# Performance work log

Hardware: AMD Instinct MI355X
Metric: run time of the kernel (lower is better)

The kernel has to match this reference:

```python
import jax, jax.numpy as jnp
import numpy as np

B, S, H = 32, 2048, 1024


def setup_inputs() -> dict:
    key = jax.random.key(0)
    ks = jax.random.split(key, 8)
    scale = 1.0 / np.sqrt(H)
    return {
        "query": jax.random.normal(ks[0], (B, 1, H), dtype=jnp.float32),
        "keys": jax.random.normal(ks[1], (B, S, H), dtype=jnp.float32),
        "Wa_w": jax.random.uniform(ks[2], (H, H), jnp.float32, -scale, scale),
        "Wa_b": jax.random.uniform(ks[3], (H,), jnp.float32, -scale, scale),
        "Ua_w": jax.random.uniform(ks[4], (H, H), jnp.float32, -scale, scale),
        "Ua_b": jax.random.uniform(ks[5], (H,), jnp.float32, -scale, scale),
        "Va_w": jax.random.uniform(ks[6], (1, H), jnp.float32, -scale, scale),
        "Va_b": jax.random.uniform(ks[7], (1,), jnp.float32, -scale, scale),
        "idx": 0,
    }


def reference(query, keys, Wa_w, Wa_b, Ua_w, Ua_b, Va_w, Va_b, idx):
    # torch Linear: y = x @ W.T + b
    q_proj = jnp.einsum("bqh,oh->bqo", query, Wa_w) + Wa_b   # (B,1,H)
    k_proj = jnp.einsum("bsh,oh->bso", keys, Ua_w) + Ua_b    # (B,S,H)
    energy = jnp.tanh(q_proj + k_proj)                        # (B,S,H) broadcast over S
    scores = jnp.einsum("bsh,h->bs", energy, Va_w[0]) + Va_b[0]  # (B,S)
    weights = jax.nn.softmax(scores, axis=-1)[:, None, :]     # (B,1,S)
    context = jnp.einsum("bqs,bsh->bqh", weights, keys)       # (B,1,H)
    return (context, weights)
```

## Files before the change

### kernel.cpp

```cpp
#include <hip/hip_runtime.h>
#include <hip/hip_bf16.h>
#include <math.h>


#define B_ 32
#define S_ 2048
#define H_ 1024
#define M_ (B_ * S_)

typedef __bf16 bf16x8 __attribute__((ext_vector_type(8)));
typedef float floatx4 __attribute__((ext_vector_type(4)));

__device__ inline unsigned bf16_rne(float f) {
  unsigned u = __builtin_bit_cast(unsigned, f);
  return (u + 0x7fffu + ((u >> 16) & 1u)) >> 16;
}
__device__ inline unsigned pk2(float x, float y) {
  return bf16_rne(x) | (bf16_rne(y) << 16);
}

#define GLDS(g, l)                                                    \
  __builtin_amdgcn_global_load_lds(                                   \
      (const __attribute__((address_space(1))) void*)(g),             \
      (__attribute__((address_space(3))) void*)(l), 16, 0, 0)

__global__ __launch_bounds__(256) void convert_kernel(
    const float* __restrict__ src, unsigned short* __restrict__ dst, int n8) {
  const int stride = gridDim.x * 256;
  for (int i = blockIdx.x * 256 + threadIdx.x; i < n8; i += stride) {
    const float4 a = ((const float4*)src)[(size_t)i * 2];
    const float4 b = ((const float4*)src)[(size_t)i * 2 + 1];
    uint4 o;
    o.x = pk2(a.x, a.y); o.y = pk2(a.z, a.w);
    o.z = pk2(b.x, b.y); o.w = pk2(b.z, b.w);
    ((uint4*)dst)[i] = o;
  }
}

__global__ __launch_bounds__(256) void qproj_kernel(
    const float* __restrict__ query, const float* __restrict__ Wa_w,
    const float* __restrict__ Wa_b, const float* __restrict__ Ua_b,
    float* __restrict__ qp) {
  const int b = blockIdx.x >> 2;
  const int os = blockIdx.x & 3;
  const int tid = threadIdx.x;
  const int lane = tid & 63;
  const int w = tid >> 6;
  __shared__ float qsh[H_];
  *(float4*)&qsh[tid * 4] = *(const float4*)(query + b * H_ + tid * 4);
  __syncthreads();
  for (int t = 0; t < 64; ++t) {
    const int o = os * 256 + w * 64 + t;
    const float* wr = Wa_w + (size_t)o * H_;
    float p = 0.f;
#pragma unroll
    for (int j = 0; j < 16; ++j) p += wr[lane + 64 * j] * qsh[lane + 64 * j];
#pragma unroll
    for (int m = 32; m; m >>= 1) p += __shfl_xor(p, m);
    if (lane == 0) qp[b * H_ + o] = p + Wa_b[o] + Ua_b[o];
  }
}

__device__ inline void swizzle_rc(int idx, int& rb, int& cb) {
  cb = (idx >> 3) & 7;
  rb = (idx & 7) | ((idx >> 6) << 3);
}

__global__ __launch_bounds__(256) void scores_bf16_kernel(
    const unsigned short* __restrict__ kbf, const unsigned short* __restrict__ ubf,
    const float* __restrict__ qp, const float* __restrict__ Va_w,
    float* __restrict__ scores) {
  const int tid = threadIdx.x;
  int rb, cb;
  swizzle_rc(blockIdx.x, rb, cb);
  const int row0 = rb * 128, c0 = cb * 128;
  const int bq = row0 >> 11;
  const int lane = tid & 63;
  const int w = tid >> 6;
  const int wm = w >> 1, wn = w & 1;
  const int q4 = lane >> 4, n16 = lane & 15;

  __shared__ __align__(16) unsigned short Asm[128][32];
  __shared__ __align__(16) unsigned short Bsm[128][32];
  __shared__ float red[2][128];

  floatx4 acc[4][4];
#pragma unroll
  for (int i = 0; i < 4; ++i)
#pragma unroll
    for (int j = 0; j < 4; ++j) acc[i][j] = {0.f, 0.f, 0.f, 0.f};

  const int r0a = w * 32;
  const int lr = lane >> 2;
  const int lc = (lane & 3) * 8;
  const unsigned short* gA0 = kbf + (size_t)(row0 + r0a + lr) * H_ + lc;
  const unsigned short* gA1 = kbf + (size_t)(row0 + r0a + 16 + lr) * H_ + lc;
  const unsigned short* gB0 = ubf + (size_t)(c0 + r0a + lr) * H_ + lc;
  const unsigned short* gB1 = ubf + (size_t)(c0 + r0a + 16 + lr) * H_ + lc;
  unsigned short* lA0 = &Asm[r0a][0];
  unsigned short* lA1 = &Asm[r0a + 16][0];
  unsigned short* lB0 = &Bsm[r0a][0];
  unsigned short* lB1 = &Bsm[r0a + 16][0];

  for (int kt = 0; kt < 32; ++kt) {
    const int k0 = kt * 32;
    __syncthreads();
    GLDS(gA0 + k0, lA0);
    GLDS(gA1 + k0, lA1);
    GLDS(gB0 + k0, lB0);
    GLDS(gB1 + k0, lB1);
    __syncthreads();
    bf16x8 af[4], bfr[4];
#pragma unroll
    for (int i = 0; i < 4; ++i)
      af[i] = *(const bf16x8*)&Asm[wm * 64 + i * 16 + n16][q4 * 8];
#pragma unroll
    for (int j = 0; j < 4; ++j)
      bfr[j] = *(const bf16x8*)&Bsm[wn * 64 + j * 16 + n16][q4 * 8];
#pragma unroll
    for (int i = 0; i < 4; ++i)
#pragma unroll
      for (int j = 0; j < 4; ++j)
        acc[i][j] = __builtin_amdgcn_mfma_f32_16x16x32_bf16(af[i], bfr[j], acc[i][j], 0, 0, 0);
  }

  float rsum[4][4];
#pragma unroll
  for (int i = 0; i < 4; ++i)
#pragma unroll
    for (int r = 0; r < 4; ++r) rsum[i][r] = 0.f;
#pragma unroll
  for (int j = 0; j < 4; ++j) {
    const int col = c0 + wn * 64 + j * 16 + n16;
    const float qv = qp[bq * H_ + col];
    const float vv = Va_w[col];
#pragma unroll
    for (int i = 0; i < 4; ++i)
#pragma unroll
      for (int r = 0; r < 4; ++r)
        rsum[i][r] += tanhf(acc[i][j][r] + qv) * vv;
  }
#pragma unroll
  for (int i = 0; i < 4; ++i)
#pragma unroll
    for (int r = 0; r < 4; ++r) {
      float v = rsum[i][r];
      v += __shfl_xor(v, 1);
      v += __shfl_xor(v, 2);
      v += __shfl_xor(v, 4);
      v += __shfl_xor(v, 8);
      rsum[i][r] = v;
    }
  if (n16 == 0) {
#pragma unroll
    for (int i = 0; i < 4; ++i)
#pragma unroll
      for (int r = 0; r < 4; ++r)
        red[wn][wm * 64 + i * 16 + q4 * 4 + r] = rsum[i][r];
  }
  __syncthreads();
  if (tid < 128) atomicAdd(scores + row0 + tid, red[0][tid] + red[1][tid]);
}

__global__ __launch_bounds__(256) void scores_f32_kernel(
    const float* __restrict__ keys, const float* __restrict__ Ua_w,
    const float* __restrict__ qp, const float* __restrict__ Va_w,
    float* __restrict__ scores) {
  const int tid = threadIdx.x;
  int rb, cb;
  swizzle_rc(blockIdx.x, rb, cb);
  const int row0 = rb * 128, c0 = cb * 128;
  const int bq = row0 >> 11;
  const int lane = tid & 63;
  const int w = tid >> 6;
  const int wm = w >> 1, wn = w & 1;
  const int q4 = lane >> 4, n16 = lane & 15;

  __shared__ __align__(16) unsigned short Asm[128][40];
  __shared__ __align__(16) unsigned short Bsm[128][40];
  __shared__ float red[2][128];

  floatx4 acc[4][4];
#pragma unroll
  for (int i = 0; i < 4; ++i)
#pragma unroll
    for (int j = 0; j < 4; ++j) acc[i][j] = {0.f, 0.f, 0.f, 0.f};

  for (int kt = 0; kt < 32; ++kt) {
    const int k0 = kt * 32;
    __syncthreads();
#pragma unroll
    for (int rep = 0; rep < 4; ++rep) {
      const int idx4 = rep * 256 + tid;
      const int r = idx4 >> 3;
      const int c4 = (idx4 & 7) << 2;
      const float4 va = *(const float4*)(keys + (size_t)(row0 + r) * H_ + k0 + c4);
      *(uint2*)&Asm[r][c4] = make_uint2(pk2(va.x, va.y), pk2(va.z, va.w));
      const float4 vb = *(const float4*)(Ua_w + (size_t)(c0 + r) * H_ + k0 + c4);
      *(uint2*)&Bsm[r][c4] = make_uint2(pk2(vb.x, vb.y), pk2(vb.z, vb.w));
    }
    __syncthreads();
    bf16x8 af[4], bfr[4];
#pragma unroll
    for (int i = 0; i < 4; ++i)
      af[i] = *(const bf16x8*)&Asm[wm * 64 + i * 16 + n16][q4 * 8];
#pragma unroll
    for (int j = 0; j < 4; ++j)
      bfr[j] = *(const bf16x8*)&Bsm[wn * 64 + j * 16 + n16][q4 * 8];
#pragma unroll
    for (int i = 0; i < 4; ++i)
#pragma unroll
      for (int j = 0; j < 4; ++j)
        acc[i][j] = __builtin_amdgcn_mfma_f32_16x16x32_bf16(af[i], bfr[j], acc[i][j], 0, 0, 0);
  }

  float rsum[4][4];
#pragma unroll
  for (int i = 0; i < 4; ++i)
#pragma unroll
    for (int r = 0; r < 4; ++r) rsum[i][r] = 0.f;
#pragma unroll
  for (int j = 0; j < 4; ++j) {
    const int col = c0 + wn * 64 + j * 16 + n16;
    const float qv = qp[bq * H_ + col];
    const float vv = Va_w[col];
#pragma unroll
    for (int i = 0; i < 4; ++i)
#pragma unroll
      for (int r = 0; r < 4; ++r)
        rsum[i][r] += tanhf(acc[i][j][r] + qv) * vv;
  }
#pragma unroll
  for (int i = 0; i < 4; ++i)
#pragma unroll
    for (int r = 0; r < 4; ++r) {
      float v = rsum[i][r];
      v += __shfl_xor(v, 1);
      v += __shfl_xor(v, 2);
      v += __shfl_xor(v, 4);
      v += __shfl_xor(v, 8);
      rsum[i][r] = v;
    }
  if (n16 == 0) {
#pragma unroll
    for (int i = 0; i < 4; ++i)
#pragma unroll
      for (int r = 0; r < 4; ++r)
        red[wn][wm * 64 + i * 16 + q4 * 4 + r] = rsum[i][r];
  }
  __syncthreads();
  if (tid < 128) atomicAdd(scores + row0 + tid, red[0][tid] + red[1][tid]);
}

__global__ __launch_bounds__(256) void softmax_kernel(float* __restrict__ sw) {
  const int b = blockIdx.x, tid = threadIdx.x;
  float v[8];
#pragma unroll
  for (int k = 0; k < 8; ++k) v[k] = sw[b * S_ + tid + 256 * k];
  float mx = v[0];
#pragma unroll
  for (int k = 1; k < 8; ++k) mx = fmaxf(mx, v[k]);
#pragma unroll
  for (int m = 32; m; m >>= 1) mx = fmaxf(mx, __shfl_xor(mx, m));
  __shared__ float sred[4], ssum[4];
  if ((tid & 63) == 0) sred[tid >> 6] = mx;
  __syncthreads();
  mx = fmaxf(fmaxf(sred[0], sred[1]), fmaxf(sred[2], sred[3]));
  float e[8], s = 0.f;
#pragma unroll
  for (int k = 0; k < 8; ++k) { e[k] = expf(v[k] - mx); s += e[k]; }
#pragma unroll
  for (int m = 32; m; m >>= 1) s += __shfl_xor(s, m);
  if ((tid & 63) == 0) ssum[tid >> 6] = s;
  __syncthreads();
  s = ssum[0] + ssum[1] + ssum[2] + ssum[3];
  const float inv = 1.0f / s;
#pragma unroll
  for (int k = 0; k < 8; ++k) sw[b * S_ + tid + 256 * k] = e[k] * inv;
}

__global__ __launch_bounds__(256) void context_kernel(
    const float* __restrict__ keys, const float* __restrict__ weights,
    float* __restrict__ ctx) {
  const int b = blockIdx.x >> 5;
  const int ch = blockIdx.x & 31;
  const int h4 = threadIdx.x * 4;
  const int s0 = ch * 64;
  const float* kp = keys + (size_t)(b * S_ + s0) * H_ + h4;
  const float* wp = weights + b * S_ + s0;
  float4 acc = {0.f, 0.f, 0.f, 0.f};
#pragma unroll 4
  for (int s = 0; s < 64; ++s) {
    const float wv = wp[s];
    const float4 kv = *(const float4*)(kp + (size_t)s * H_);
    acc.x += wv * kv.x; acc.y += wv * kv.y; acc.z += wv * kv.z; acc.w += wv * kv.w;
  }
  atomicAdd(ctx + b * H_ + h4 + 0, acc.x);
  atomicAdd(ctx + b * H_ + h4 + 1, acc.y);
  atomicAdd(ctx + b * H_ + h4 + 2, acc.z);
  atomicAdd(ctx + b * H_ + h4 + 3, acc.w);
}

extern "C" void kernel_launch(void* const* d_in, const int* in_sizes, int n_in,
                              void* d_out, int out_size, void* d_ws, size_t ws_size,
                              hipStream_t stream) {
  const float* query = (const float*)d_in[0];
  const float* keys  = (const float*)d_in[1];
  const float* Wa_w  = (const float*)d_in[2];
  const float* Wa_b  = (const float*)d_in[3];
  const float* Ua_w  = (const float*)d_in[4];
  const float* Ua_b  = (const float*)d_in[5];
  const float* Va_w  = (const float*)d_in[6];

  float* out = (float*)d_out;
  float* ctx = out;
  float* sw  = out + B_ * H_;

  const size_t kb  = (size_t)M_ * H_ * 2;
  const size_t ub  = (size_t)H_ * H_ * 2;
  const size_t qpb = (size_t)B_ * H_ * 4;
  const bool fast = ws_size >= kb + ub + qpb;

  (void)hipMemsetAsync(d_out, 0, (size_t)out_size * sizeof(float), stream);

  if (fast) {
    unsigned short* kbf = (unsigned short*)d_ws;
    unsigned short* ubf = (unsigned short*)((char*)d_ws + kb);
    float* qp = (float*)((char*)d_ws + kb + ub);
    convert_kernel<<<2048, 256, 0, stream>>>(keys, kbf, M_ * H_ / 8);
    convert_kernel<<<256, 256, 0, stream>>>(Ua_w, ubf, H_ * H_ / 8);
    qproj_kernel<<<128, 256, 0, stream>>>(query, Wa_w, Wa_b, Ua_b, qp);
    scores_bf16_kernel<<<4096, 256, 0, stream>>>(kbf, ubf, qp, Va_w, sw);
  } else {
    float* qp = (float*)d_ws;
    qproj_kernel<<<128, 256, 0, stream>>>(query, Wa_w, Wa_b, Ua_b, qp);
    scores_f32_kernel<<<4096, 256, 0, stream>>>(keys, Ua_w, qp, Va_w, sw);
  }
  softmax_kernel<<<B_, 256, 0, stream>>>(sw);
  context_kernel<<<1024, 256, 0, stream>>>(keys, sw, ctx);
}
```

Measured before the change: 748.9 us.

## Swizzle LDS tiles, use fast tanh, rework qproj and two-stage context reduction

XOR-swizzles the 16-byte chunk placement in the bf16 GEMM's LDS tiles so the MFMA operand reads hit fewer bank conflicts. Replaces tanhf with a clamped exp/reciprocal approximation to cut transcendental cost in the epilogue. Rewrites qproj so each thread computes one output with float4 loads. Replaces the atomic context accumulation with per-chunk partials followed by a second reduction kernel. The workspace layout changes; the fast tanh trades some accuracy, and the extra kernel and partial buffer add launch and memory traffic.

```diff
diff --git a/kernel.cpp b/kernel.cpp
--- a/kernel.cpp
+++ b/kernel.cpp
@@ -17,6 +17,12 @@
 }
 __device__ inline unsigned pk2(float x, float y) {
   return bf16_rne(x) | (bf16_rne(y) << 16);
+}
+
+__device__ inline float fast_tanh(float x) {
+  const float xc = fminf(fmaxf(x, -8.f), 8.f);
+  const float e = __expf(2.f * xc);
+  return (e - 1.f) * __builtin_amdgcn_rcpf(e + 1.f);
 }
 
 #define GLDS(g, l)                                                    \
@@ -41,30 +47,26 @@
     const float* __restrict__ query, const float* __restrict__ Wa_w,
     const float* __restrict__ Wa_b, const float* __restrict__ Ua_b,
     float* __restrict__ qp) {
-  const int b = blockIdx.x >> 2;
-  const int os = blockIdx.x & 3;
-  const int tid = threadIdx.x;
-  const int lane = tid & 63;
-  const int w = tid >> 6;
-  __shared__ float qsh[H_];
-  *(float4*)&qsh[tid * 4] = *(const float4*)(query + b * H_ + tid * 4);
-  __syncthreads();
-  for (int t = 0; t < 64; ++t) {
-    const int o = os * 256 + w * 64 + t;
-    const float* wr = Wa_w + (size_t)o * H_;
-    float p = 0.f;
-#pragma unroll
-    for (int j = 0; j < 16; ++j) p += wr[lane + 64 * j] * qsh[lane + 64 * j];
-#pragma unroll
-    for (int m = 32; m; m >>= 1) p += __shfl_xor(p, m);
-    if (lane == 0) qp[b * H_ + o] = p + Wa_b[o] + Ua_b[o];
-  }
+  const int g = blockIdx.x * 256 + threadIdx.x;
+  const int b = g & 31;
+  const int o = g >> 5;
+  const float4* wr = (const float4*)(Wa_w + (size_t)o * H_);
+  const float4* qr = (const float4*)(query + (size_t)b * H_);
+  float4 s4 = {0.f, 0.f, 0.f, 0.f};
+#pragma unroll 8
+  for (int k = 0; k < 256; ++k) {
+    const float4 w = wr[k], q = qr[k];
+    s4.x += w.x * q.x; s4.y += w.y * q.y; s4.z += w.z * q.z; s4.w += w.w * q.w;
+  }
+  qp[b * H_ + o] = (s4.x + s4.y) + (s4.z + s4.w) + Wa_b[o] + Ua_b[o];
 }
 
 __device__ inline void swizzle_rc(int idx, int& rb, int& cb) {
   cb = (idx >> 3) & 7;
   rb = (idx & 7) | ((idx >> 6) << 3);
 }
+
+__device__ inline int chunk_f(int r) { return (r & 3) ^ ((r >> 2) & 3); }
 
 __global__ __launch_bounds__(256) void scores_bf16_kernel(
     const unsigned short* __restrict__ kbf, const unsigned short* __restrict__ ubf,
@@ -92,7 +94,7 @@
 
   const int r0a = w * 32;
   const int lr = lane >> 2;
-  const int lc = (lane & 3) * 8;
+  const int lc = ((lane & 3) ^ chunk_f(lr)) * 8;
   const unsigned short* gA0 = kbf + (size_t)(row0 + r0a + lr) * H_ + lc;
   const unsigned short* gA1 = kbf + (size_t)(row0 + r0a + 16 + lr) * H_ + lc;
   const unsigned short* gB0 = ubf + (size_t)(c0 + r0a + lr) * H_ + lc;
@@ -101,6 +103,8 @@
   unsigned short* lA1 = &Asm[r0a + 16][0];
   unsigned short* lB0 = &Bsm[r0a][0];
   unsigned short* lB1 = &Bsm[r0a + 16][0];
+
+  const int fn = chunk_f(n16);
 
   for (int kt = 0; kt < 32; ++kt) {
     const int k0 = kt * 32;
@@ -113,10 +117,10 @@
     bf16x8 af[4], bfr[4];
 #pragma unroll
     for (int i = 0; i < 4; ++i)
-      af[i] = *(const bf16x8*)&Asm[wm * 64 + i * 16 + n16][q4 * 8];
+      af[i] = *(const bf16x8*)&Asm[wm * 64 + i * 16 + n16][(q4 ^ fn) * 8];
 #pragma unroll
     for (int j = 0; j < 4; ++j)
-      bfr[j] = *(const bf16x8*)&Bsm[wn * 64 + j * 16 + n16][q4 * 8];
+      bfr[j] = *(const bf16x8*)&Bsm[wn * 64 + j * 16 + n16][(q4 ^ fn) * 8];
 #pragma unroll
     for (int i = 0; i < 4; ++i)
 #pragma unroll
@@ -138,7 +142,7 @@
     for (int i = 0; i < 4; ++i)
 #pragma unroll
       for (int r = 0; r < 4; ++r)
-        rsum[i][r] += tanhf(acc[i][j][r] + qv) * vv;
+        rsum[i][r] += fast_tanh(acc[i][j][r] + qv) * vv;
   }
 #pragma unroll
   for (int i = 0; i < 4; ++i)
@@ -228,7 +232,7 @@
     for (int i = 0; i < 4; ++i)
 #pragma unroll
       for (int r = 0; r < 4; ++r)
-        rsum[i][r] += tanhf(acc[i][j][r] + qv) * vv;
+        rsum[i][r] += fast_tanh(acc[i][j][r] + qv) * vv;
   }
 #pragma unroll
   for (int i = 0; i < 4; ++i)
@@ -279,7 +283,39 @@
   for (int k = 0; k < 8; ++k) sw[b * S_ + tid + 256 * k] = e[k] * inv;
 }
 
-__global__ __launch_bounds__(256) void context_kernel(
+__global__ __launch_bounds__(256) void context1_kernel(
+    const float* __restrict__ keys, const float* __restrict__ weights,
+    float* __restrict__ pctx) {
+  const int b = blockIdx.x >> 5;
+  const int ch = blockIdx.x & 31;
+  const int h4 = threadIdx.x * 4;
+  const int s0 = ch * 64;
+  const float* kp = keys + (size_t)(b * S_ + s0) * H_ + h4;
+  const float* wp = weights + b * S_ + s0;
+  float4 acc = {0.f, 0.f, 0.f, 0.f};
+#pragma unroll 4
+  for (int s = 0; s < 64; ++s) {
+    const float wv = wp[s];
+    const float4 kv = *(const float4*)(kp + (size_t)s * H_);
+    acc.x += wv * kv.x; acc.y += wv * kv.y; acc.z += wv * kv.z; acc.w += wv * kv.w;
+  }
+  *(float4*)(pctx + ((size_t)(b * 32 + ch)) * H_ + h4) = acc;
+}
+
+__global__ __launch_bounds__(256) void context2_kernel(
+    const float* __restrict__ pctx, float* __restrict__ ctx) {
+  const int b = blockIdx.x;
+  const int h4 = threadIdx.x * 4;
+  float4 acc = {0.f, 0.f, 0.f, 0.f};
+#pragma unroll 8
+  for (int c = 0; c < 32; ++c) {
+    const float4 v = *(const float4*)(pctx + ((size_t)(b * 32 + c)) * H_ + h4);
+    acc.x += v.x; acc.y += v.y; acc.z += v.z; acc.w += v.w;
+  }
+  *(float4*)(ctx + b * H_ + h4) = acc;
+}
+
+__global__ __launch_bounds__(256) void context_atomic_kernel(
     const float* __restrict__ keys, const float* __restrict__ weights,
     float* __restrict__ ctx) {
   const int b = blockIdx.x >> 5;
@@ -316,26 +352,32 @@
   float* ctx = out;
   float* sw  = out + B_ * H_;
 
-  const size_t kb  = (size_t)M_ * H_ * 2;
-  const size_t ub  = (size_t)H_ * H_ * 2;
-  const size_t qpb = (size_t)B_ * H_ * 4;
-  const bool fast = ws_size >= kb + ub + qpb;
+  const size_t qpb  = (size_t)B_ * H_ * 4;
+  const size_t pcb  = (size_t)B_ * 32 * H_ * 4;
+  const size_t kb   = (size_t)M_ * H_ * 2;
+  const size_t ub   = (size_t)H_ * H_ * 2;
+  float* qp = (float*)d_ws;
+  float* pctx = (float*)((char*)d_ws + qpb);
+  unsigned short* kbf = (unsigned short*)((char*)d_ws + qpb + pcb);
+  unsigned short* ubf = (unsigned short*)((char*)d_ws + qpb + pcb + kb);
+  const bool fast = ws_size >= qpb + pcb + kb + ub;
+  const bool twostage = ws_size >= qpb + pcb;
 
   (void)hipMemsetAsync(d_out, 0, (size_t)out_size * sizeof(float), stream);
 
+  qproj_kernel<<<128, 256, 0, stream>>>(query, Wa_w, Wa_b, Ua_b, qp);
   if (fast) {
-    unsigned short* kbf = (unsigned short*)d_ws;
-    unsigned short* ubf = (unsigned short*)((char*)d_ws + kb);
-    float* qp = (float*)((char*)d_ws + kb + ub);
     convert_kernel<<<2048, 256, 0, stream>>>(keys, kbf, M_ * H_ / 8);
     convert_kernel<<<256, 256, 0, stream>>>(Ua_w, ubf, H_ * H_ / 8);
-    qproj_kernel<<<128, 256, 0, stream>>>(query, Wa_w, Wa_b, Ua_b, qp);
     scores_bf16_kernel<<<4096, 256, 0, stream>>>(kbf, ubf, qp, Va_w, sw);
   } else {
-    float* qp = (float*)d_ws;
-    qproj_kernel<<<128, 256, 0, stream>>>(query, Wa_w, Wa_b, Ua_b, qp);
     scores_f32_kernel<<<4096, 256, 0, stream>>>(keys, Ua_w, qp, Va_w, sw);
   }
   softmax_kernel<<<B_, 256, 0, stream>>>(sw);
-  context_kernel<<<1024, 256, 0, stream>>>(keys, sw, ctx);
-}
+  if (twostage) {
+    context1_kernel<<<1024, 256, 0, stream>>>(keys, sw, pctx);
+    context2_kernel<<<B_, 256, 0, stream>>>(pctx, ctx);
+  } else {
+    context_atomic_kernel<<<1024, 256, 0, stream>>>(keys, sw, ctx);
+  }
+}
```

Result: faster. 664.7 us (-11.2%).

## Fuse prep kernels, swizzle LDS, fast tanh, replace atomics with partial buffers

Applied to the files above, without the earlier changes.

Merges the keys/Ua conversion and q-projection into one prep kernel launch. Adds an XOR swizzle to the LDS layout to reduce bank conflicts, and replaces tanhf/expf with cheaper exp-plus-reciprocal approximations. Score and context atomics become writes to partial buffers that are reduced later: in softmax for scores, and in a new second context kernel for the context. This removes the memset and atomic contention but needs more workspace and one extra launch, and loses a little tanh accuracy.

```diff
diff --git a/kernel.cpp b/kernel.cpp
--- a/kernel.cpp
+++ b/kernel.cpp
@@ -8,6 +8,10 @@
 #define H_ 1024
 #define M_ (B_ * S_)
 
+#define CONV_BLOCKS 8192
+#define UA_BLOCKS 32
+#define QP_BLOCKS 512
+
 typedef __bf16 bf16x8 __attribute__((ext_vector_type(8)));
 typedef float floatx4 __attribute__((ext_vector_type(4)));
 
@@ -17,6 +21,12 @@
 }
 __device__ inline unsigned pk2(float x, float y) {
   return bf16_rne(x) | (bf16_rne(y) << 16);
+}
+
+__device__ inline float fast_tanh(float x) {
+  const float xc = fminf(fmaxf(x, -8.f), 8.f);
+  const float e = __expf(2.f * xc);
+  return (e - 1.f) * __builtin_amdgcn_rcpf(e + 1.f);
 }
 
 #define GLDS(g, l)                                                    \
@@ -24,40 +34,57 @@
       (const __attribute__((address_space(1))) void*)(g),             \
       (__attribute__((address_space(3))) void*)(l), 16, 0, 0)
 
-__global__ __launch_bounds__(256) void convert_kernel(
-    const float* __restrict__ src, unsigned short* __restrict__ dst, int n8) {
-  const int stride = gridDim.x * 256;
-  for (int i = blockIdx.x * 256 + threadIdx.x; i < n8; i += stride) {
-    const float4 a = ((const float4*)src)[(size_t)i * 2];
-    const float4 b = ((const float4*)src)[(size_t)i * 2 + 1];
-    uint4 o;
-    o.x = pk2(a.x, a.y); o.y = pk2(a.z, a.w);
-    o.z = pk2(b.x, b.y); o.w = pk2(b.z, b.w);
-    ((uint4*)dst)[i] = o;
-  }
-}
-
-__global__ __launch_bounds__(256) void qproj_kernel(
+__device__ inline uint4 conv8(const float4* s2) {
+  const float4 a = s2[0], b = s2[1];
+  uint4 o;
+  o.x = pk2(a.x, a.y); o.y = pk2(a.z, a.w);
+  o.z = pk2(b.x, b.y); o.w = pk2(b.z, b.w);
+  return o;
+}
+
+__global__ __launch_bounds__(256) void prep_kernel(
+    const float* __restrict__ keys, const float* __restrict__ Ua_w,
     const float* __restrict__ query, const float* __restrict__ Wa_w,
     const float* __restrict__ Wa_b, const float* __restrict__ Ua_b,
-    float* __restrict__ qp) {
-  const int b = blockIdx.x >> 2;
-  const int os = blockIdx.x & 3;
+    unsigned short* __restrict__ kbf, unsigned short* __restrict__ ubf,
+    float* __restrict__ qp, int do_convert) {
+  const int blk = blockIdx.x;
   const int tid = threadIdx.x;
-  const int lane = tid & 63;
-  const int w = tid >> 6;
-  __shared__ float qsh[H_];
-  *(float4*)&qsh[tid * 4] = *(const float4*)(query + b * H_ + tid * 4);
-  __syncthreads();
-  for (int t = 0; t < 64; ++t) {
-    const int o = os * 256 + w * 64 + t;
-    const float* wr = Wa_w + (size_t)o * H_;
-    float p = 0.f;
-#pragma unroll
-    for (int j = 0; j < 16; ++j) p += wr[lane + 64 * j] * qsh[lane + 64 * j];
-#pragma unroll
-    for (int m = 32; m; m >>= 1) p += __shfl_xor(p, m);
-    if (lane == 0) qp[b * H_ + o] = p + Wa_b[o] + Ua_b[o];
+  if (blk < CONV_BLOCKS) {
+    if (!do_convert) return;
+    const int tg = blk * 256 + tid;
+#pragma unroll
+    for (int c = 0; c < 4; ++c) {
+      const size_t idx = (size_t)c * 2097152 + tg;
+      ((uint4*)kbf)[idx] = conv8((const float4*)keys + idx * 2);
+    }
+  } else if (blk < CONV_BLOCKS + UA_BLOCKS) {
+    if (!do_convert) return;
+    const int tg = (blk - CONV_BLOCKS) * 256 + tid;
+#pragma unroll
+    for (int c = 0; c < 16; ++c) {
+      const size_t idx = (size_t)c * 8192 + tg;
+      ((uint4*)ubf)[idx] = conv8((const float4*)Ua_w + idx * 2);
+    }
+  } else {
+    const int bl = blk - CONV_BLOCKS - UA_BLOCKS;
+    const int b = bl >> 4;
+    const int os = (bl & 15) * 64;
+    const int lane = tid & 63;
+    const int w = tid >> 6;
+    __shared__ float qsh[H_];
+    *(float4*)&qsh[tid * 4] = *(const float4*)(query + (size_t)b * H_ + tid * 4);
+    __syncthreads();
+    for (int t = 0; t < 16; ++t) {
+      const int o = os + w * 16 + t;
+      const float* wr = Wa_w + (size_t)o * H_;
+      float p = 0.f;
+#pragma unroll
+      for (int j = 0; j < 16; ++j) p += wr[lane + 64 * j] * qsh[lane + 64 * j];
+#pragma unroll
+      for (int m = 32; m; m >>= 1) p += __shfl_xor(p, m);
+      if (lane == 0) qp[b * H_ + o] = p + Wa_b[o] + Ua_b[o];
+    }
   }
 }
 
@@ -65,11 +92,12 @@
   cb = (idx >> 3) & 7;
   rb = (idx & 7) | ((idx >> 6) << 3);
 }
+__device__ inline int chunk_f(int r) { return (r & 3) ^ ((r >> 2) & 3); }
 
 __global__ __launch_bounds__(256) void scores_bf16_kernel(
     const unsigned short* __restrict__ kbf, const unsigned short* __restrict__ ubf,
     const float* __restrict__ qp, const float* __restrict__ Va_w,
-    float* __restrict__ scores) {
+    float* __restrict__ sp) {
   const int tid = threadIdx.x;
   int rb, cb;
   swizzle_rc(blockIdx.x, rb, cb);
@@ -92,7 +120,7 @@
 
   const int r0a = w * 32;
   const int lr = lane >> 2;
-  const int lc = (lane & 3) * 8;
+  const int lc = ((lane & 3) ^ chunk_f(lr)) * 8;
   const unsigned short* gA0 = kbf + (size_t)(row0 + r0a + lr) * H_ + lc;
   const unsigned short* gA1 = kbf + (size_t)(row0 + r0a + 16 + lr) * H_ + lc;
   const unsigned short* gB0 = ubf + (size_t)(c0 + r0a + lr) * H_ + lc;
@@ -102,6 +130,8 @@
   unsigned short* lB0 = &Bsm[r0a][0];
   unsigned short* lB1 = &Bsm[r0a + 16][0];
 
+  const int fn = chunk_f(n16);
+
   for (int kt = 0; kt < 32; ++kt) {
     const int k0 = kt * 32;
     __syncthreads();
@@ -113,10 +143,10 @@
     bf16x8 af[4], bfr[4];
 #pragma unroll
     for (int i = 0; i < 4; ++i)
-      af[i] = *(const bf16x8*)&Asm[wm * 64 + i * 16 + n16][q4 * 8];
+      af[i] = *(const bf16x8*)&Asm[wm * 64 + i * 16 + n16][(q4 ^ fn) * 8];
 #pragma unroll
     for (int j = 0; j < 4; ++j)
-      bfr[j] = *(const bf16x8*)&Bsm[wn * 64 + j * 16 + n16][q4 * 8];
+      bfr[j] = *(const bf16x8*)&Bsm[wn * 64 + j * 16 + n16][(q4 ^ fn) * 8];
 #pragma unroll
     for (int i = 0; i < 4; ++i)
 #pragma unroll
@@ -138,7 +168,7 @@
     for (int i = 0; i < 4; ++i)
 #pragma unroll
       for (int r = 0; r < 4; ++r)
-        rsum[i][r] += tanhf(acc[i][j][r] + qv) * vv;
+        rsum[i][r] += fast_tanh(acc[i][j][r] + qv) * vv;
   }
 #pragma unroll
   for (int i = 0; i < 4; ++i)
@@ -159,13 +189,13 @@
         red[wn][wm * 64 + i * 16 + q4 * 4 + r] = rsum[i][r];
   }
   __syncthreads();
-  if (tid < 128) atomicAdd(scores + row0 + tid, red[0][tid] + red[1][tid]);
+  if (tid < 128) sp[(size_t)cb * M_ + row0 + tid] = red[0][tid] + red[1][tid];
 }
 
 __global__ __launch_bounds__(256) void scores_f32_kernel(
     const float* __restrict__ keys, const float* __restrict__ Ua_w,
     const float* __restrict__ qp, const float* __restrict__ Va_w,
-    float* __restrict__ scores) {
+    float* __restrict__ sp) {
   const int tid = threadIdx.x;
   int rb, cb;
   swizzle_rc(blockIdx.x, rb, cb);
@@ -228,7 +258,7 @@
     for (int i = 0; i < 4; ++i)
 #pragma unroll
       for (int r = 0; r < 4; ++r)
-        rsum[i][r] += tanhf(acc[i][j][r] + qv) * vv;
+        rsum[i][r] += fast_tanh(acc[i][j][r] + qv) * vv;
   }
 #pragma unroll
   for (int i = 0; i < 4; ++i)
@@ -249,14 +279,21 @@
         red[wn][wm * 64 + i * 16 + q4 * 4 + r] = rsum[i][r];
   }
   __syncthreads();
-  if (tid < 128) atomicAdd(scores + row0 + tid, red[0][tid] + red[1][tid]);
-}
-
-__global__ __launch_bounds__(256) void softmax_kernel(float* __restrict__ sw) {
+  if (tid < 128) sp[(size_t)cb * M_ + row0 + tid] = red[0][tid] + red[1][tid];
+}
+
+__global__ __launch_bounds__(256) void softmax_kernel(
+    const float* __restrict__ sp, float* __restrict__ sw) {
   const int b = blockIdx.x, tid = threadIdx.x;
   float v[8];
 #pragma unroll
-  for (int k = 0; k < 8; ++k) v[k] = sw[b * S_ + tid + 256 * k];
+  for (int k = 0; k < 8; ++k) {
+    const size_t base = (size_t)b * S_ + tid + 256 * k;
+    float s = 0.f;
+#pragma unroll
+    for (int j = 0; j < 8; ++j) s += sp[(size_t)j * M_ + base];
+    v[k] = s;
+  }
   float mx = v[0];
 #pragma unroll
   for (int k = 1; k < 8; ++k) mx = fmaxf(mx, v[k]);
@@ -268,7 +305,7 @@
   mx = fmaxf(fmaxf(sred[0], sred[1]), fmaxf(sred[2], sred[3]));
   float e[8], s = 0.f;
 #pragma unroll
-  for (int k = 0; k < 8; ++k) { e[k] = expf(v[k] - mx); s += e[k]; }
+  for (int k = 0; k < 8; ++k) { e[k] = __expf(v[k] - mx); s += e[k]; }
 #pragma unroll
   for (int m = 32; m; m >>= 1) s += __shfl_xor(s, m);
   if ((tid & 63) == 0) ssum[tid >> 6] = s;
@@ -279,26 +316,42 @@
   for (int k = 0; k < 8; ++k) sw[b * S_ + tid + 256 * k] = e[k] * inv;
 }
 
-__global__ __launch_bounds__(256) void context_kernel(
+__global__ __launch_bounds__(256) void context1_kernel(
     const float* __restrict__ keys, const float* __restrict__ weights,
-    float* __restrict__ ctx) {
-  const int b = blockIdx.x >> 5;
-  const int ch = blockIdx.x & 31;
+    float* __restrict__ pctx) {
+  const int b = blockIdx.x >> 6;
+  const int ch = blockIdx.x & 63;
+  const int s0 = ch * 32;
+  const int h4 = threadIdx.x;
+  const float4* kp4 = (const float4*)(keys + (size_t)(b * S_ + s0) * H_) + h4;
+  const float4* wp4 = (const float4*)(weights + b * S_ + s0);
+  float4 acc = {0.f, 0.f, 0.f, 0.f};
+#pragma unroll
+  for (int sq = 0; sq < 8; ++sq) {
+    const float4 wv = wp4[sq];
+    const float4 k0 = kp4[(sq * 4 + 0) * 256];
+    const float4 k1 = kp4[(sq * 4 + 1) * 256];
+    const float4 k2 = kp4[(sq * 4 + 2) * 256];
+    const float4 k3 = kp4[(sq * 4 + 3) * 256];
+    acc.x += wv.x * k0.x + wv.y * k1.x + wv.z * k2.x + wv.w * k3.x;
+    acc.y += wv.x * k0.y + wv.y * k1.y + wv.z * k2.y + wv.w * k3.y;
+    acc.z += wv.x * k0.z + wv.y * k1.z + wv.z * k2.z + wv.w * k3.z;
+    acc.w += wv.x * k0.w + wv.y * k1.w + wv.z * k2.w + wv.w * k3.w;
+  }
+  *(float4*)(pctx + ((size_t)(b * 64 + ch)) * H_ + h4 * 4) = acc;
+}
+
+__global__ __launch_bounds__(256) void context2_kernel(
+    const float* __restrict__ pctx, float* __restrict__ ctx) {
+  const int b = blockIdx.x;
   const int h4 = threadIdx.x * 4;
-  const int s0 = ch * 64;
-  const float* kp = keys + (size_t)(b * S_ + s0) * H_ + h4;
-  const float* wp = weights + b * S_ + s0;
   float4 acc = {0.f, 0.f, 0.f, 0.f};
-#pragma unroll 4
-  for (int s = 0; s < 64; ++s) {
-    const float wv = wp[s];
-    const float4 kv = *(const float4*)(kp + (size_t)s * H_);
-    acc.x += wv * kv.x; acc.y += wv * kv.y; acc.z += wv * kv.z; acc.w += wv * kv.w;
-  }
-  atomicAdd(ctx + b * H_ + h4 + 0, acc.x);
-  atomicAdd(ctx + b * H_ + h4 + 1, acc.y);
-  atomicAdd(ctx + b * H_ + h4 + 2, acc.z);
-  atomicAdd(ctx + b * H_ + h4 + 3, acc.w);
+#pragma unroll 8
+  for (int c = 0; c < 64; ++c) {
+    const float4 v = *(const float4*)(pctx + ((size_t)(b * 64 + c)) * H_ + h4);
+    acc.x += v.x; acc.y += v.y; acc.z += v.z; acc.w += v.w;
+  }
+  *(float4*)(ctx + b * H_ + h4) = acc;
 }
 
 extern "C" void kernel_launch(void* const* d_in, const int* in_sizes, int n_in,
@@ -316,26 +369,26 @@
   float* ctx = out;
   float* sw  = out + B_ * H_;
 
+  const size_t qpb = (size_t)B_ * H_ * 4;
+  const size_t spb = (size_t)8 * M_ * 4;
+  const size_t pcb = (size_t)B_ * 64 * H_ * 4;
   const size_t kb  = (size_t)M_ * H_ * 2;
   const size_t ub  = (size_t)H_ * H_ * 2;
-  const size_t qpb = (size_t)B_ * H_ * 4;
-  const bool fast = ws_size >= kb + ub + qpb;
-
-  (void)hipMemsetAsync(d_out, 0, (size_t)out_size * sizeof(float), stream);
-
+  float* qp = (float*)d_ws;
+  float* sp = (float*)((char*)d_ws + qpb);
+  float* pctx = (float*)((char*)d_ws + qpb + spb);
+  unsigned short* kbf = (unsigned short*)((char*)d_ws + qpb + spb + pcb);
+  unsigned short* ubf = (unsigned short*)((char*)d_ws + qpb + spb + pcb + kb);
+  const bool fast = ws_size >= qpb + spb + pcb + kb + ub;
+
+  prep_kernel<<<CONV_BLOCKS + UA_BLOCKS + QP_BLOCKS, 256, 0, stream>>>(
+      keys, Ua_w, query, Wa_w, Wa_b, Ua_b, kbf, ubf, qp, fast ? 1 : 0);
   if (fast) {
-    unsigned short* kbf = (unsigned short*)d_ws;
-    unsigned short* ubf = (unsigned short*)((char*)d_ws + kb);
-    float* qp = (float*)((char*)d_ws + kb + ub);
-    convert_kernel<<<2048, 256, 0, stream>>>(keys, kbf, M_ * H_ / 8);
-    convert_kernel<<<256, 256, 0, stream>>>(Ua_w, ubf, H_ * H_ / 8);
-    qproj_kernel<<<128, 256, 0, stream>>>(query, Wa_w, Wa_b, Ua_b, qp);
-    scores_bf16_kernel<<<4096, 256, 0, stream>>>(kbf, ubf, qp, Va_w, sw);
+    scores_bf16_kernel<<<4096, 256, 0, stream>>>(kbf, ubf, qp, Va_w, sp);
   } else {
-    float* qp = (float*)d_ws;
-    qproj_kernel<<<128, 256, 0, stream>>>(query, Wa_w, Wa_b, Ua_b, qp);
-    scores_f32_kernel<<<4096, 256, 0, stream>>>(keys, Ua_w, qp, Va_w, sw);
-  }
-  softmax_kernel<<<B_, 256, 0, stream>>>(sw);
-  context_kernel<<<1024, 256, 0, stream>>>(keys, sw, ctx);
-}
+    scores_f32_kernel<<<4096, 256, 0, stream>>>(keys, Ua_w, qp, Va_w, sp);
+  }
+  softmax_kernel<<<B_, 256, 0, stream>>>(sp, sw);
+  context1_kernel<<<2048, 256, 0, stream>>>(keys, sw, pctx);
+  context2_kernel<<<B_, 256, 0, stream>>>(pctx, ctx);
+}
```

After: 629.9 us. -15.9%, faster.
